# Kernel optimization log

Hardware: AMD Instinct MI355X
Metric: run time of the kernel (lower is better)

## Reference

```python
import jax, jax.numpy as jnp
import numpy as np

N_GENOMES = 30000
N_GENES = 240000
N_SAMPLES = 128
N_SEQS = 80000


def setup_inputs() -> dict:
    key = jax.random.key(0)
    k0, k1, k2, k3, k4 = jax.random.split(key, 5)
    A = jax.random.normal(k0, (N_GENOMES, N_SAMPLES), dtype=jnp.float32)  # log-abundance
    B = jax.random.normal(k1, (N_GENOMES, N_SAMPLES), dtype=jnp.float32)  # log-PTR
    pos = jax.random.uniform(k2, (N_GENES,), dtype=jnp.float32)           # dist from ori, in [0,1)
    genome_idx = jnp.sort(jax.random.randint(k3, (N_GENES,), 0, N_GENOMES))  # block one-hot of `members`
    seq_idx = jax.random.randint(k4, (N_GENES,), 0, N_SEQS)               # gene -> md5 sequence map
    return {"A": A, "B": B, "pos": pos, "genome_idx": genome_idx, "seq_idx": seq_idx}


def reference(A, B, pos, genome_idx, seq_idx):
    # G = members @ A + 1 - dists @ B, where members/dists are one-hot per gene row
    # -> gather rows of A and B by genome assignment, scale B row by gene position.
    G = A[genome_idx] + 1.0 - pos[:, None] * B[genome_idx]   # (m, s)
    # gene_to_seq @ exp(G) -> segment sum of exp(G) over gene->sequence assignment
    return jax.ops.segment_sum(jnp.exp(G), seq_idx, num_segments=N_SEQS)  # (k, s)
```

## Files before the change

### kernel.cpp

```cpp
#include <hip/hip_runtime.h>

#define N_GENOMES 30000
#define N_GENES   240000
#define N_SAMPLES 128
#define N_SEQS    80000
#define CAP       32

__global__ __launch_bounds__(256) void scatter_kernel(
    const int*   __restrict__ seq_idx,
    const int*   __restrict__ genome_idx,
    const float* __restrict__ pos,
    int*         __restrict__ cnt,
    int2*        __restrict__ bucket)
{
    int gene = blockIdx.x * blockDim.x + threadIdx.x;
    if (gene >= N_GENES) return;
    int s = seq_idx[gene];
    int2 rec;
    rec.x = genome_idx[gene];
    rec.y = __float_as_int(pos[gene]);
    int slot = atomicAdd(&cnt[s], 1);
    if (slot < CAP) bucket[s * CAP + slot] = rec;
}

__global__ __launch_bounds__(256) void accum_kernel(
    const float* __restrict__ A,
    const float* __restrict__ B,
    const int*   __restrict__ cnt,
    const int2*  __restrict__ bucket,
    float*       __restrict__ out)
{
    int idx  = blockIdx.x * blockDim.x + threadIdx.x;
    int seq  = idx >> 5;
    int quad = idx & 31;
    if (seq >= N_SEQS) return;

    int n = cnt[seq];
    if (n > CAP) n = CAP;

    const int2* bk = bucket + seq * CAP;
    const float4* A4 = reinterpret_cast<const float4*>(A);
    const float4* B4 = reinterpret_cast<const float4*>(B);

    float4 acc = make_float4(0.f, 0.f, 0.f, 0.f);

    for (int i0 = 0; i0 < n; i0 += 4) {
        int2   r[4];
        int    g[4];
        float  p[4];
        bool   live[4];
        float4 a[4], b[4];

        #pragma unroll
        for (int j = 0; j < 4; ++j) {
            live[j] = (i0 + j) < n;
            r[j] = bk[i0 + j];
        }
        #pragma unroll
        for (int j = 0; j < 4; ++j) {
            g[j] = live[j] ? r[j].x : 0;
            p[j] = __int_as_float(r[j].y);
        }
        #pragma unroll
        for (int j = 0; j < 4; ++j) {
            a[j] = A4[g[j] * 32 + quad];
            b[j] = B4[g[j] * 32 + quad];
        }
        #pragma unroll
        for (int j = 0; j < 4; ++j) {
            float4 e;
            e.x = __expf(a[j].x + 1.0f - p[j] * b[j].x);
            e.y = __expf(a[j].y + 1.0f - p[j] * b[j].y);
            e.z = __expf(a[j].z + 1.0f - p[j] * b[j].z);
            e.w = __expf(a[j].w + 1.0f - p[j] * b[j].w);
            if (live[j]) {
                acc.x += e.x; acc.y += e.y; acc.z += e.z; acc.w += e.w;
            }
        }
    }

    reinterpret_cast<float4*>(out)[seq * 32 + quad] = acc;
}

extern "C" void kernel_launch(void* const* d_in, const int* in_sizes, int n_in,
                              void* d_out, int out_size, void* d_ws, size_t ws_size,
                              hipStream_t stream) {
    const float* A    = (const float*)d_in[0];
    const float* B    = (const float*)d_in[1];
    const float* pos  = (const float*)d_in[2];
    const int*   gidx = (const int*)d_in[3];
    const int*   sidx = (const int*)d_in[4];
    float*       out  = (float*)d_out;

    int*  cnt    = (int*)d_ws;
    int2* bucket = (int2*)(cnt + N_SEQS);

    hipMemsetAsync(cnt, 0, N_SEQS * sizeof(int), stream);

    scatter_kernel<<<(N_GENES + 255) / 256, 256, 0, stream>>>(
        sidx, gidx, pos, cnt, bucket);

    const int total = N_SEQS * 32;
    accum_kernel<<<(total + 255) / 256, 256, 0, stream>>>(
        A, B, cnt, bucket, out);
}
```

Measured before the change: 132.4 us.

## Pack A and B into interleaved fp16 and compress bucket records to 32 bits

A prep pass converts A (with the +1 folded in) and B into one interleaved half-precision table, so each gathered gene row costs one 16-byte load instead of two. Bucket records shrink from int2 to a single 32-bit word holding a 15-bit genome index and a 17-bit quantized position. The scatter and the compression now run in one merged launch. This reduces gather traffic in the accumulation kernel, at the cost of an extra pass over A and B each call and lower precision from fp16 values and quantized positions.

```diff
diff --git a/kernel.cpp b/kernel.cpp
--- a/kernel.cpp
+++ b/kernel.cpp
@@ -1,4 +1,5 @@
 #include <hip/hip_runtime.h>
+#include <hip/hip_fp16.h>
 
 #define N_GENOMES 30000
 #define N_GENES   240000
@@ -6,29 +7,48 @@
 #define N_SEQS    80000
 #define CAP       32
 
-__global__ __launch_bounds__(256) void scatter_kernel(
+#define SCATTER_BLOCKS  ((N_GENES + 255) / 256)
+#define COMPRESS_BLOCKS ((N_GENOMES * 32 + 255) / 256)
+
+__global__ __launch_bounds__(256) void prep_kernel(
+    const float* __restrict__ A,
+    const float* __restrict__ B,
+    const float* __restrict__ pos,
+    const int*   __restrict__ genome_idx,
     const int*   __restrict__ seq_idx,
-    const int*   __restrict__ genome_idx,
-    const float* __restrict__ pos,
-    int*         __restrict__ cnt,
-    int2*        __restrict__ bucket)
+    int*          __restrict__ cnt,
+    unsigned int* __restrict__ bucket,
+    float4*       __restrict__ AB16)
 {
-    int gene = blockIdx.x * blockDim.x + threadIdx.x;
-    if (gene >= N_GENES) return;
-    int s = seq_idx[gene];
-    int2 rec;
-    rec.x = genome_idx[gene];
-    rec.y = __float_as_int(pos[gene]);
-    int slot = atomicAdd(&cnt[s], 1);
-    if (slot < CAP) bucket[s * CAP + slot] = rec;
+    int b = blockIdx.x;
+    if (b < SCATTER_BLOCKS) {
+        int gene = b * 256 + threadIdx.x;
+        if (gene >= N_GENES) return;
+        int   s = seq_idx[gene];
+        int   g = genome_idx[gene];
+        float p = pos[gene];
+        unsigned int q   = (unsigned int)(p * 131072.0f);
+        unsigned int rec = (unsigned int)g | (q << 15);
+        int slot = atomicAdd(&cnt[s], 1);
+        if (slot < CAP) bucket[s * CAP + slot] = rec;
+    } else {
+        int idx = (b - SCATTER_BLOCKS) * 256 + threadIdx.x;
+        const float4 a  = reinterpret_cast<const float4*>(A)[idx];
+        const float4 bb = reinterpret_cast<const float4*>(B)[idx];
+        __half2 h[4];
+        h[0] = __floats2half2_rn(a.x + 1.0f, a.y + 1.0f);
+        h[1] = __floats2half2_rn(a.z + 1.0f, a.w + 1.0f);
+        h[2] = __floats2half2_rn(bb.x, bb.y);
+        h[3] = __floats2half2_rn(bb.z, bb.w);
+        AB16[idx] = *reinterpret_cast<float4*>(h);
+    }
 }
 
 __global__ __launch_bounds__(256) void accum_kernel(
-    const float* __restrict__ A,
-    const float* __restrict__ B,
-    const int*   __restrict__ cnt,
-    const int2*  __restrict__ bucket,
-    float*       __restrict__ out)
+    const float4*       __restrict__ AB16,
+    const int*          __restrict__ cnt,
+    const unsigned int* __restrict__ bucket,
+    float*              __restrict__ out)
 {
     int idx  = blockIdx.x * blockDim.x + threadIdx.x;
     int seq  = idx >> 5;
@@ -38,18 +58,14 @@
     int n = cnt[seq];
     if (n > CAP) n = CAP;
 
-    const int2* bk = bucket + seq * CAP;
-    const float4* A4 = reinterpret_cast<const float4*>(A);
-    const float4* B4 = reinterpret_cast<const float4*>(B);
-
+    const unsigned int* bk = bucket + seq * CAP;
     float4 acc = make_float4(0.f, 0.f, 0.f, 0.f);
 
     for (int i0 = 0; i0 < n; i0 += 4) {
-        int2   r[4];
-        int    g[4];
-        float  p[4];
-        bool   live[4];
-        float4 a[4], b[4];
+        unsigned int r[4];
+        float        p[4];
+        bool         live[4];
+        float4       raw[4];
 
         #pragma unroll
         for (int j = 0; j < 4; ++j) {
@@ -58,21 +74,26 @@
         }
         #pragma unroll
         for (int j = 0; j < 4; ++j) {
-            g[j] = live[j] ? r[j].x : 0;
-            p[j] = __int_as_float(r[j].y);
+            if (!live[j]) r[j] = 0;
+            p[j] = (float)(r[j] >> 15) * (1.0f / 131072.0f);
         }
         #pragma unroll
         for (int j = 0; j < 4; ++j) {
-            a[j] = A4[g[j] * 32 + quad];
-            b[j] = B4[g[j] * 32 + quad];
+            int g = (int)(r[j] & 0x7fffu);
+            raw[j] = AB16[g * 32 + quad];
         }
         #pragma unroll
         for (int j = 0; j < 4; ++j) {
+            const __half2* hp = reinterpret_cast<const __half2*>(&raw[j]);
+            float2 a01 = __half22float2(hp[0]);
+            float2 a23 = __half22float2(hp[1]);
+            float2 b01 = __half22float2(hp[2]);
+            float2 b23 = __half22float2(hp[3]);
             float4 e;
-            e.x = __expf(a[j].x + 1.0f - p[j] * b[j].x);
-            e.y = __expf(a[j].y + 1.0f - p[j] * b[j].y);
-            e.z = __expf(a[j].z + 1.0f - p[j] * b[j].z);
-            e.w = __expf(a[j].w + 1.0f - p[j] * b[j].w);
+            e.x = __expf(a01.x - p[j] * b01.x);
+            e.y = __expf(a01.y - p[j] * b01.y);
+            e.z = __expf(a23.x - p[j] * b23.x);
+            e.w = __expf(a23.y - p[j] * b23.y);
             if (live[j]) {
                 acc.x += e.x; acc.y += e.y; acc.z += e.z; acc.w += e.w;
             }
@@ -92,15 +113,17 @@
     const int*   sidx = (const int*)d_in[4];
     float*       out  = (float*)d_out;
 
-    int*  cnt    = (int*)d_ws;
-    int2* bucket = (int2*)(cnt + N_SEQS);
+    char*         ws     = (char*)d_ws;
+    float4*       AB16   = (float4*)ws;
+    int*          cnt    = (int*)(ws + (size_t)N_GENOMES * 32 * 16);
+    unsigned int* bucket = (unsigned int*)(cnt + N_SEQS);
 
     hipMemsetAsync(cnt, 0, N_SEQS * sizeof(int), stream);
 
-    scatter_kernel<<<(N_GENES + 255) / 256, 256, 0, stream>>>(
-        sidx, gidx, pos, cnt, bucket);
+    prep_kernel<<<SCATTER_BLOCKS + COMPRESS_BLOCKS, 256, 0, stream>>>(
+        A, B, pos, gidx, sidx, cnt, bucket, AB16);
 
     const int total = N_SEQS * 32;
     accum_kernel<<<(total + 255) / 256, 256, 0, stream>>>(
-        A, B, cnt, bucket, out);
+        AB16, cnt, bucket, out);
 }
```

Result: faster. 125.7 us (-5.0%).
